# Performance work log

Hardware: AMD Instinct MI355X
Metric: run time of the kernel (lower is better)

## Reference

```python
import jax, jax.numpy as jnp
import numpy as np

# Synaptic (snntorch) constants: alpha = exp(-dt/tau_s), beta = exp(-dt/tau_m)
DT, TAU_S, TAU_M = 1.0, 5.0, 10.0
ALPHA = float(np.exp(-DT / TAU_S))
BETA = float(np.exp(-DT / TAU_M))
THRESH = 1.0


def heaviside(u):
    return (u > 0).astype(u.dtype)


def setup_inputs() -> dict:
    key = jax.random.key(0)
    k1, k2 = jax.random.split(key)
    T, B, D1, D2 = 128, 256, 1024, 512
    inp = jax.random.uniform(k1, (T, B, D1), dtype=jnp.float32)
    # kaiming_normal_ on [d2, d1] (fan_in = d1), then * mu (=1.0)
    w = jax.random.normal(k2, (D2, D1), dtype=jnp.float32) * np.float32(np.sqrt(2.0 / D1))
    return {"input": inp, "weight": w}


def reference(input, weight):
    T, B = input.shape[0], input.shape[1]
    D2 = weight.shape[0]
    # step i (i=1..T-1) consumes F.linear(input[i-1], W); batch all GEMMs at once
    cur = jnp.einsum('tbi,oi->tbo', input[:-1], weight)  # [T-1, B, D2]

    def step(carry, c):
        syn, mem = carry
        reset = heaviside(mem - THRESH)          # spike from previous membrane
        syn = ALPHA * syn + c                    # synaptic current decay + drive
        mem = (BETA * mem + syn) * (1.0 - reset)  # zero-reset membrane update
        spk = heaviside(mem - THRESH)
        return (syn, mem), (spk, mem, syn)

    zeros = jnp.zeros((B, D2), input.dtype)
    _, (spk, V, I) = jax.lax.scan(step, (zeros, zeros), cur)

    z0 = jnp.zeros((1, B, D2), input.dtype)  # outputs at t=0 stay zero
    output = jnp.concatenate([z0, spk], axis=0)
    V = jnp.concatenate([z0, V], axis=0)
    I = jnp.concatenate([z0, I], axis=0)
    return output, V, I
```

## Files before the change

kernel.cpp:

```cpp
#include <hip/hip_runtime.h>
#include <cstddef>

#define TT 128
#define BB 256
#define D1 1024
#define D2 512
#define SS (BB * D2)
#define MM (127 * BB)

#define ALPHA 0.8187307530779818f
#define BETA  0.9048374180359595f

typedef _Float16 half8 __attribute__((ext_vector_type(8)));
typedef _Float16 half4v __attribute__((ext_vector_type(4)));
typedef float floatx16 __attribute__((ext_vector_type(16)));

__global__ __launch_bounds__(256) void convert_w(const float* __restrict__ W,
                                                 _Float16* __restrict__ Whi,
                                                 _Float16* __restrict__ Wlo) {
    const int i = (blockIdx.x * 256 + threadIdx.x) * 4;
    float4 w = *(const float4*)(W + i);
    half4v hi, lo;
    hi.x = (_Float16)w.x; lo.x = (_Float16)((w.x - (float)hi.x) * 2048.0f);
    hi.y = (_Float16)w.y; lo.y = (_Float16)((w.y - (float)hi.y) * 2048.0f);
    hi.z = (_Float16)w.z; lo.z = (_Float16)((w.z - (float)hi.z) * 2048.0f);
    hi.w = (_Float16)w.w; lo.w = (_Float16)((w.w - (float)hi.w) * 2048.0f);
    *(half4v*)(Whi + i) = hi;
    *(half4v*)(Wlo + i) = lo;
}

#define BM 64
#define BN 256
#define BK 32
#define LDH 48

__global__ __launch_bounds__(256, 2) void gemm_mfma(const float* __restrict__ A,
                                                    const _Float16* __restrict__ Whi,
                                                    const _Float16* __restrict__ Wlo,
                                                    float* __restrict__ C) {
    __shared__ _Float16 Ah[BM * LDH];
    __shared__ _Float16 Al[BM * LDH];
    __shared__ _Float16 Wh[BN * LDH];
    __shared__ _Float16 Wl[BN * LDH];

    const int tid = threadIdx.x;
    const int lane = tid & 63;
    const int wv = tid >> 6;
    const int bm = blockIdx.x * BM;
    const int bn = blockIdx.y * BN;

    const int arow = tid >> 2;
    const int kch = (tid & 3) * 8;

    const int m_ = lane & 31;
    const int q = lane >> 5;

    floatx16 accm[2][2], accl[2][2];
#pragma unroll
    for (int i = 0; i < 2; ++i)
#pragma unroll
        for (int j = 0; j < 2; ++j) {
            accm[i][j] = (floatx16)0.0f;
            accl[i][j] = (floatx16)0.0f;
        }

    const float* Abase = A + (size_t)(bm + arow) * D1 + kch;

    for (int k0 = 0; k0 < D1; k0 += BK) {
        float4 a0 = *(const float4*)(Abase + k0);
        float4 a1 = *(const float4*)(Abase + k0 + 4);
        half8 wh[4], wl[4];
#pragma unroll
        for (int p = 0; p < 4; ++p) {
            const int wr = bn + p * 64 + arow;
            wh[p] = *(const half8*)(Whi + wr * D1 + k0 + kch);
            wl[p] = *(const half8*)(Wlo + wr * D1 + k0 + kch);
        }

        __syncthreads();

        float av[8] = {a0.x, a0.y, a0.z, a0.w, a1.x, a1.y, a1.z, a1.w};
        half8 ah, al;
#pragma unroll
        for (int j = 0; j < 8; ++j) {
            _Float16 h = (_Float16)av[j];
            ah[j] = h;
            al[j] = (_Float16)((av[j] - (float)h) * 2048.0f);
        }
        *(half8*)&Ah[arow * LDH + kch] = ah;
        *(half8*)&Al[arow * LDH + kch] = al;
#pragma unroll
        for (int p = 0; p < 4; ++p) {
            *(half8*)&Wh[(p * 64 + arow) * LDH + kch] = wh[p];
            *(half8*)&Wl[(p * 64 + arow) * LDH + kch] = wl[p];
        }
        __syncthreads();

#pragma unroll
        for (int kk = 0; kk < BK; kk += 16) {
            const int ko = kk + q * 8;
            half8 a_hi[2], a_lo[2], b_hi[2], b_lo[2];
#pragma unroll
            for (int mb = 0; mb < 2; ++mb) {
                a_hi[mb] = *(const half8*)&Ah[(mb * 32 + m_) * LDH + ko];
                a_lo[mb] = *(const half8*)&Al[(mb * 32 + m_) * LDH + ko];
            }
#pragma unroll
            for (int nb = 0; nb < 2; ++nb) {
                b_hi[nb] = *(const half8*)&Wh[(wv * 64 + nb * 32 + m_) * LDH + ko];
                b_lo[nb] = *(const half8*)&Wl[(wv * 64 + nb * 32 + m_) * LDH + ko];
            }
#pragma unroll
            for (int mb = 0; mb < 2; ++mb)
#pragma unroll
                for (int nb = 0; nb < 2; ++nb) {
                    accm[mb][nb] = __builtin_amdgcn_mfma_f32_32x32x16_f16(
                        a_hi[mb], b_hi[nb], accm[mb][nb], 0, 0, 0);
                    accl[mb][nb] = __builtin_amdgcn_mfma_f32_32x32x16_f16(
                        a_hi[mb], b_lo[nb], accl[mb][nb], 0, 0, 0);
                    accl[mb][nb] = __builtin_amdgcn_mfma_f32_32x32x16_f16(
                        a_lo[mb], b_hi[nb], accl[mb][nb], 0, 0, 0);
                }
        }
    }

#pragma unroll
    for (int mb = 0; mb < 2; ++mb)
#pragma unroll
        for (int nb = 0; nb < 2; ++nb) {
            const int n = bn + wv * 64 + nb * 32 + m_;
#pragma unroll
            for (int reg = 0; reg < 16; ++reg) {
                const int row = (reg & 3) + 8 * (reg >> 2) + 4 * q;
                const int m = bm + mb * 32 + row;
                C[m * D2 + n] = accm[mb][nb][reg] + accl[mb][nb][reg] * (1.0f / 2048.0f);
            }
        }
}

__global__ __launch_bounds__(256) void scan_kernel(float* __restrict__ out) {
    const int j = blockIdx.x * 256 + threadIdx.x;
    float* spk = out;
    float* V = out + TT * SS;
    float* I = out + 2 * TT * SS;

    spk[j] = 0.0f;
    V[j] = 0.0f;
    I[j] = 0.0f;

    float syn = 0.0f, mem = 0.0f;

#define STEP(tt, cc)                                     \
    {                                                    \
        const float reset = (mem > 1.0f) ? 1.0f : 0.0f;  \
        syn = ALPHA * syn + (cc);                        \
        mem = (BETA * mem + syn) * (1.0f - reset);       \
        const int idx = (tt) * SS + j;                   \
        spk[idx] = (mem > 1.0f) ? 1.0f : 0.0f;           \
        V[idx] = mem;                                    \
        I[idx] = syn;                                    \
    }

    float c0 = I[1 * SS + j];
    float c1 = I[2 * SS + j];
    float c2 = I[3 * SS + j];
    float c3 = I[4 * SS + j];

    int t = 1;
    for (; t <= 117; t += 4) {
        const float n0 = I[(t + 4) * SS + j];
        const float n1 = I[(t + 5) * SS + j];
        const float n2 = I[(t + 6) * SS + j];
        const float n3 = I[(t + 7) * SS + j];
        STEP(t + 0, c0);
        STEP(t + 1, c1);
        STEP(t + 2, c2);
        STEP(t + 3, c3);
        c0 = n0; c1 = n1; c2 = n2; c3 = n3;
    }
    {
        const float n0 = I[125 * SS + j];
        const float n1 = I[126 * SS + j];
        const float n2 = I[127 * SS + j];
        STEP(121, c0);
        STEP(122, c1);
        STEP(123, c2);
        STEP(124, c3);
        STEP(125, n0);
        STEP(126, n1);
        STEP(127, n2);
    }
#undef STEP
}

extern "C" void kernel_launch(void* const* d_in, const int* in_sizes, int n_in,
                              void* d_out, int out_size, void* d_ws, size_t ws_size,
                              hipStream_t stream) {
    const float* input = (const float*)d_in[0];
    const float* weight = (const float*)d_in[1];
    float* out = (float*)d_out;

    _Float16* Whi = (_Float16*)(out + SS);
    _Float16* Wlo = Whi + (size_t)D2 * D1;

    float* Cdst = out + (size_t)2 * TT * SS + SS;

    convert_w<<<dim3((D2 * D1 / 4) / 256), dim3(256), 0, stream>>>(weight, Whi, Wlo);
    gemm_mfma<<<dim3(MM / BM, D2 / BN), dim3(256), 0, stream>>>(input, Whi, Wlo, Cdst);
    scan_kernel<<<dim3(SS / 256), dim3(256), 0, stream>>>(out);
}
```

Measured before the change: 411.0 us.

## Pre-swizzle weights to MFMA fragment layout and double-buffer GEMM with direct LDS loads

The weight conversion now writes the fp16 hi/lo splits in an MFMA-fragment-tiled order. The GEMM can then copy them straight into LDS with global_load_lds, skipping the register round trip. The GEMM moves to 128x128 tiles with 8 waves, double-buffered LDS, register prefetch of A two steps ahead, one barrier per K step, and setprio around the MFMA groups. The aim is to overlap global loads with MFMA work and cut per-iteration synchronization. In exchange the schedule relies on hand-tuned waitcnt values and a fixed-shape layout, which makes it fragile.

After: 391.7 us. -4.7%, faster.

```diff
diff --git a/kernel.cpp b/kernel.cpp
--- a/kernel.cpp
+++ b/kernel.cpp
@@ -1,5 +1,6 @@
 #include <hip/hip_runtime.h>
 #include <cstddef>
+#include <cstdint>
 
 #define TT 128
 #define BB 256
@@ -12,130 +13,165 @@
 #define BETA  0.9048374180359595f
 
 typedef _Float16 half8 __attribute__((ext_vector_type(8)));
-typedef _Float16 half4v __attribute__((ext_vector_type(4)));
 typedef float floatx16 __attribute__((ext_vector_type(16)));
 
 __global__ __launch_bounds__(256) void convert_w(const float* __restrict__ W,
                                                  _Float16* __restrict__ Whi,
                                                  _Float16* __restrict__ Wlo) {
-    const int i = (blockIdx.x * 256 + threadIdx.x) * 4;
-    float4 w = *(const float4*)(W + i);
-    half4v hi, lo;
-    hi.x = (_Float16)w.x; lo.x = (_Float16)((w.x - (float)hi.x) * 2048.0f);
-    hi.y = (_Float16)w.y; lo.y = (_Float16)((w.y - (float)hi.y) * 2048.0f);
-    hi.z = (_Float16)w.z; lo.z = (_Float16)((w.z - (float)hi.z) * 2048.0f);
-    hi.w = (_Float16)w.w; lo.w = (_Float16)((w.w - (float)hi.w) * 2048.0f);
-    *(half4v*)(Whi + i) = hi;
-    *(half4v*)(Wlo + i) = lo;
-}
-
-#define BM 64
-#define BN 256
-#define BK 32
-#define LDH 48
-
-__global__ __launch_bounds__(256, 2) void gemm_mfma(const float* __restrict__ A,
+    const int T = blockIdx.x * 256 + threadIdx.x;
+    const int l = T & 63;
+    const int ch = (T >> 6) & 7;
+    const int nB = (T >> 9) & 3;
+    const int kt = T >> 11;
+    const int row = nB * 128 + (ch & 3) * 32 + (l & 31);
+    const int k = kt * 32 + (ch >> 2) * 16 + (l >> 5) * 8;
+    const float* src = W + (size_t)row * D1 + k;
+    float4 w0 = *(const float4*)src;
+    float4 w1 = *(const float4*)(src + 4);
+    float f[8] = {w0.x, w0.y, w0.z, w0.w, w1.x, w1.y, w1.z, w1.w};
+    half8 hi, lo;
+#pragma unroll
+    for (int j = 0; j < 8; ++j) {
+        _Float16 h = (_Float16)f[j];
+        hi[j] = h;
+        lo[j] = (_Float16)((f[j] - (float)h) * 2048.0f);
+    }
+    *(half8*)(Whi + (size_t)T * 8) = hi;
+    *(half8*)(Wlo + (size_t)T * 8) = lo;
+}
+
+#define GLOAD16(gp, lp)                                                        \
+    __builtin_amdgcn_global_load_lds(                                          \
+        (const __attribute__((address_space(1))) void*)(gp),                   \
+        (__attribute__((address_space(3))) void*)(lp), 16, 0, 0)
+
+__global__ __launch_bounds__(512, 2) void gemm_mfma(const float* __restrict__ A,
                                                     const _Float16* __restrict__ Whi,
                                                     const _Float16* __restrict__ Wlo,
                                                     float* __restrict__ C) {
-    __shared__ _Float16 Ah[BM * LDH];
-    __shared__ _Float16 Al[BM * LDH];
-    __shared__ _Float16 Wh[BN * LDH];
-    __shared__ _Float16 Wl[BN * LDH];
+    __shared__ _Float16 lds[2][4][4096];
 
     const int tid = threadIdx.x;
     const int lane = tid & 63;
-    const int wv = tid >> 6;
-    const int bm = blockIdx.x * BM;
-    const int bn = blockIdx.y * BN;
-
-    const int arow = tid >> 2;
-    const int kch = (tid & 3) * 8;
-
+    const int w = tid >> 6;
+    const int wm = w >> 2;
+    const int wn = w & 3;
+    const int bm = blockIdx.x * 128;
+    const int nB = blockIdx.y;
+    const int bn = nB * 128;
     const int m_ = lane & 31;
     const int q = lane >> 5;
 
-    floatx16 accm[2][2], accl[2][2];
+    const int o_ = tid & 3;
+    const int r0 = tid >> 2;
+    const int chA = ((o_ >> 1) << 2) + (r0 >> 5);
+    const int sA = chA * 512 + ((o_ & 1) * 32 + (r0 & 31)) * 8;
+    const float* Ab0 = A + (size_t)(bm + r0) * D1 + o_ * 8;
+
+    const _Float16* WsrcH = Whi + (size_t)nB * 4096 + w * 512 + lane * 8;
+    const _Float16* WsrcL = Wlo + (size_t)nB * 4096 + w * 512 + lane * 8;
+
+    const int fA0 = (wm * 2 + 0) * 512 + lane * 8;
+    const int fA1 = (wm * 2 + 1) * 512 + lane * 8;
+    const int fB = wn * 512 + lane * 8;
+
+    floatx16 accm[2], accl[2];
+    accm[0] = (floatx16)0.0f; accm[1] = (floatx16)0.0f;
+    accl[0] = (floatx16)0.0f; accl[1] = (floatx16)0.0f;
+
+    float4 ra0, ra1;
+    float4 rb0, rb1;
+
+#define STAGE_A(BUF, F0, F1)                                                   \
+    {                                                                          \
+        float fv[8] = {F0.x, F0.y, F0.z, F0.w, F1.x, F1.y, F1.z, F1.w};        \
+        half8 hh, ll;                                                          \
+        _Pragma("unroll")                                                      \
+        for (int u = 0; u < 8; ++u) {                                          \
+            _Float16 hv = (_Float16)fv[u];                                     \
+            hh[u] = hv;                                                        \
+            ll[u] = (_Float16)((fv[u] - (float)hv) * 2048.0f);                 \
+        }                                                                      \
+        *(half8*)&lds[BUF][0][sA] = hh;                                        \
+        *(half8*)&lds[BUF][1][sA] = ll;                                        \
+    }
+
+#define MFMA6(BUF, KS)                                                         \
+    {                                                                          \
+        const half8 ah0 = *(const half8*)&lds[BUF][0][fA0 + (KS)*2048];        \
+        const half8 ah1 = *(const half8*)&lds[BUF][0][fA1 + (KS)*2048];        \
+        const half8 al0 = *(const half8*)&lds[BUF][1][fA0 + (KS)*2048];        \
+        const half8 al1 = *(const half8*)&lds[BUF][1][fA1 + (KS)*2048];        \
+        const half8 bh = *(const half8*)&lds[BUF][2][fB + (KS)*2048];          \
+        const half8 bl = *(const half8*)&lds[BUF][3][fB + (KS)*2048];          \
+        accm[0] = __builtin_amdgcn_mfma_f32_32x32x16_f16(ah0, bh, accm[0], 0, 0, 0); \
+        accl[0] = __builtin_amdgcn_mfma_f32_32x32x16_f16(ah0, bl, accl[0], 0, 0, 0); \
+        accl[0] = __builtin_amdgcn_mfma_f32_32x32x16_f16(al0, bh, accl[0], 0, 0, 0); \
+        accm[1] = __builtin_amdgcn_mfma_f32_32x32x16_f16(ah1, bh, accm[1], 0, 0, 0); \
+        accl[1] = __builtin_amdgcn_mfma_f32_32x32x16_f16(ah1, bl, accl[1], 0, 0, 0); \
+        accl[1] = __builtin_amdgcn_mfma_f32_32x32x16_f16(al1, bh, accl[1], 0, 0, 0); \
+    }
+
+#define BODY(JT, BUF, C0, C1, N0, N1, PREF_A, VMN)                             \
+    {                                                                          \
+        asm volatile("" ::: "memory");                 \
+        GLOAD16(WsrcH + (size_t)((JT) + 1) * 16384, &lds[(BUF) ^ 1][2][w * 512]); \
+        GLOAD16(WsrcL + (size_t)((JT) + 1) * 16384, &lds[(BUF) ^ 1][3][w * 512]); \
+        __builtin_amdgcn_sched_barrier(0);     \
+        if (PREF_A) {                                                          \
+            const int kf = ((JT) + 2) * 32;                                    \
+            N0 = *(const float4*)(Ab0 + kf);                                   \
+            N1 = *(const float4*)(Ab0 + kf + 4);                               \
+        }                                                                      \
+        STAGE_A((BUF) ^ 1, C0, C1);                                            \
+        __builtin_amdgcn_s_setprio(1);                                         \
+        MFMA6(BUF, 0);                                                         \
+        __builtin_amdgcn_s_setprio(0);                                         \
+        __builtin_amdgcn_s_setprio(1);                                         \
+        MFMA6(BUF, 1);                                                         \
+        __builtin_amdgcn_s_setprio(0);                                         \
+        asm volatile("s_waitcnt vmcnt(" #VMN ") lgkmcnt(0)" ::: "memory");     \
+        __builtin_amdgcn_s_barrier();                                          \
+    }
+
+    GLOAD16(WsrcH, &lds[0][2][w * 512]);
+    GLOAD16(WsrcL, &lds[0][3][w * 512]);
+    __builtin_amdgcn_sched_barrier(0);
+    ra0 = *(const float4*)(Ab0);
+    ra1 = *(const float4*)(Ab0 + 4);
+    rb0 = *(const float4*)(Ab0 + 32);
+    rb1 = *(const float4*)(Ab0 + 36);
+    STAGE_A(0, ra0, ra1);
+    asm volatile("s_waitcnt vmcnt(2) lgkmcnt(0)" ::: "memory");
+    __builtin_amdgcn_s_barrier();
+
+    for (int jj = 0; jj < 30; jj += 2) {
+        BODY(jj, 0, rb0, rb1, ra0, ra1, 1, 2)
+        BODY(jj + 1, 1, ra0, ra1, rb0, rb1, 1, 2)
+    }
+    BODY(30, 0, rb0, rb1, ra0, ra1, 0, 0)
+    asm volatile("" ::: "memory");
+    __builtin_amdgcn_s_setprio(1);
+    MFMA6(1, 0);
+    __builtin_amdgcn_s_setprio(0);
+    __builtin_amdgcn_s_setprio(1);
+    MFMA6(1, 1);
+    __builtin_amdgcn_s_setprio(0);
+
+#undef BODY
+#undef MFMA6
+#undef STAGE_A
+
+    const int n = bn + wn * 32 + m_;
 #pragma unroll
-    for (int i = 0; i < 2; ++i)
+    for (int mb = 0; mb < 2; ++mb) {
 #pragma unroll
-        for (int j = 0; j < 2; ++j) {
-            accm[i][j] = (floatx16)0.0f;
-            accl[i][j] = (floatx16)0.0f;
+        for (int reg = 0; reg < 16; ++reg) {
+            const int row = (reg & 3) + 8 * (reg >> 2) + 4 * q;
+            const int m = bm + wm * 64 + mb * 32 + row;
+            C[(size_t)m * D2 + n] = accm[mb][reg] + accl[mb][reg] * (1.0f / 2048.0f);
         }
-
-    const float* Abase = A + (size_t)(bm + arow) * D1 + kch;
-
-    for (int k0 = 0; k0 < D1; k0 += BK) {
-        float4 a0 = *(const float4*)(Abase + k0);
-        float4 a1 = *(const float4*)(Abase + k0 + 4);
-        half8 wh[4], wl[4];
-#pragma unroll
-        for (int p = 0; p < 4; ++p) {
-            const int wr = bn + p * 64 + arow;
-            wh[p] = *(const half8*)(Whi + wr * D1 + k0 + kch);
-            wl[p] = *(const half8*)(Wlo + wr * D1 + k0 + kch);
-        }
-
-        __syncthreads();
-
-        float av[8] = {a0.x, a0.y, a0.z, a0.w, a1.x, a1.y, a1.z, a1.w};
-        half8 ah, al;
-#pragma unroll
-        for (int j = 0; j < 8; ++j) {
-            _Float16 h = (_Float16)av[j];
-            ah[j] = h;
-            al[j] = (_Float16)((av[j] - (float)h) * 2048.0f);
-        }
-        *(half8*)&Ah[arow * LDH + kch] = ah;
-        *(half8*)&Al[arow * LDH + kch] = al;
-#pragma unroll
-        for (int p = 0; p < 4; ++p) {
-            *(half8*)&Wh[(p * 64 + arow) * LDH + kch] = wh[p];
-            *(half8*)&Wl[(p * 64 + arow) * LDH + kch] = wl[p];
-        }
-        __syncthreads();
-
-#pragma unroll
-        for (int kk = 0; kk < BK; kk += 16) {
-            const int ko = kk + q * 8;
-            half8 a_hi[2], a_lo[2], b_hi[2], b_lo[2];
-#pragma unroll
-            for (int mb = 0; mb < 2; ++mb) {
-                a_hi[mb] = *(const half8*)&Ah[(mb * 32 + m_) * LDH + ko];
-                a_lo[mb] = *(const half8*)&Al[(mb * 32 + m_) * LDH + ko];
-            }
-#pragma unroll
-            for (int nb = 0; nb < 2; ++nb) {
-                b_hi[nb] = *(const half8*)&Wh[(wv * 64 + nb * 32 + m_) * LDH + ko];
-                b_lo[nb] = *(const half8*)&Wl[(wv * 64 + nb * 32 + m_) * LDH + ko];
-            }
-#pragma unroll
-            for (int mb = 0; mb < 2; ++mb)
-#pragma unroll
-                for (int nb = 0; nb < 2; ++nb) {
-                    accm[mb][nb] = __builtin_amdgcn_mfma_f32_32x32x16_f16(
-                        a_hi[mb], b_hi[nb], accm[mb][nb], 0, 0, 0);
-                    accl[mb][nb] = __builtin_amdgcn_mfma_f32_32x32x16_f16(
-                        a_hi[mb], b_lo[nb], accl[mb][nb], 0, 0, 0);
-                    accl[mb][nb] = __builtin_amdgcn_mfma_f32_32x32x16_f16(
-                        a_lo[mb], b_hi[nb], accl[mb][nb], 0, 0, 0);
-                }
-        }
-    }
-
-#pragma unroll
-    for (int mb = 0; mb < 2; ++mb)
-#pragma unroll
-        for (int nb = 0; nb < 2; ++nb) {
-            const int n = bn + wv * 64 + nb * 32 + m_;
-#pragma unroll
-            for (int reg = 0; reg < 16; ++reg) {
-                const int row = (reg & 3) + 8 * (reg >> 2) + 4 * q;
-                const int m = bm + mb * 32 + row;
-                C[m * D2 + n] = accm[mb][nb][reg] + accl[mb][nb][reg] * (1.0f / 2048.0f);
-            }
-        }
+    }
 }
 
 __global__ __launch_bounds__(256) void scan_kernel(float* __restrict__ out) {
@@ -205,7 +241,7 @@
 
     float* Cdst = out + (size_t)2 * TT * SS + SS;
 
-    convert_w<<<dim3((D2 * D1 / 4) / 256), dim3(256), 0, stream>>>(weight, Whi, Wlo);
-    gemm_mfma<<<dim3(MM / BM, D2 / BN), dim3(256), 0, stream>>>(input, Whi, Wlo, Cdst);
+    convert_w<<<dim3((D2 * D1 / 8) / 256), dim3(256), 0, stream>>>(weight, Whi, Wlo);
+    gemm_mfma<<<dim3(MM / 128, D2 / 128), dim3(512), 0, stream>>>(input, Whi, Wlo, Cdst);
     scan_kernel<<<dim3(SS / 256), dim3(256), 0, stream>>>(out);
 }
```
